# Optimization experiments

Measured on AMD Instinct MI355X. Metric: run time of the kernel, lower is better.

The kernel has to match this reference:

```python
import jax, jax.numpy as jnp
import numpy as np

B, T, V, H = 16, 256, 64, 256  # batch, time, num_inputs, hidden_dim
EPS = 1e-5

def _layernorm(h, g, b):
    mu = jnp.mean(h, axis=-1, keepdims=True)
    var = jnp.mean(jnp.square(h - mu), axis=-1, keepdims=True)
    return (h - mu) * jax.lax.rsqrt(var + EPS) * g + b

def setup_inputs() -> dict:
    key = jax.random.key(0)
    ks = jax.random.split(key, 16)
    s1, sH = 1.0, 1.0 / np.sqrt(H)
    sV = 1.0 / np.sqrt(V)
    inp = {
        "x": jax.random.normal(ks[0], (B, T, V), jnp.float32),
        # per-variable GRN params (input_dim=1), stacked over V
        "W1": jax.random.normal(ks[1], (V, H), jnp.float32) * s1,
        "b1": jnp.zeros((V, H), jnp.float32),
        "W2": jax.random.normal(ks[2], (V, H, H), jnp.float32) * sH,
        "b2": jnp.zeros((V, H), jnp.float32),
        "Wg": jax.random.normal(ks[3], (V, H), jnp.float32) * s1,  # first H rows of gate Linear(1,2H)
        "bg": jnp.zeros((V, H), jnp.float32),
        "Ws": jax.random.normal(ks[4], (V, H), jnp.float32) * s1,  # skip_proj Linear(1,H)
        "bs": jnp.zeros((V, H), jnp.float32),
        "g1": jnp.ones((V, H), jnp.float32),
        "be1": jnp.zeros((V, H), jnp.float32),
        # weight network GRN: V -> V, skip is Identity
        "nW1": jax.random.normal(ks[5], (V, V), jnp.float32) * sV,
        "nb1": jnp.zeros((V,), jnp.float32),
        "nW2": jax.random.normal(ks[6], (V, V), jnp.float32) * sV,
        "nb2": jnp.zeros((V,), jnp.float32),
        "nWg": jax.random.normal(ks[7], (V, V), jnp.float32) * sV,  # first V cols of gate Linear(V,2V)
        "nbg": jnp.zeros((V,), jnp.float32),
        "ng": jnp.ones((V,), jnp.float32),
        "nbe": jnp.zeros((V,), jnp.float32),
    }
    return inp

def reference(x, W1, b1, W2, b2, Wg, bg, Ws, bs, g1, be1,
              nW1, nb1, nW2, nb2, nWg, nbg, ng, nbe):
    # --- per-variable GRNs, vectorized over V (input is a scalar per variable) ---
    feat = x[..., None]                                     # [B,T,V,1]
    h1 = feat * W1 + b1                                     # [B,T,V,H]  fc1(1->H)
    res = jnp.einsum('btvh,vhk->btvk', jax.nn.elu(h1), W2) + b2  # fc2(H->H)
    gate = jax.nn.sigmoid(feat * Wg + bg)                   # gate(1->2H)[:H]
    skip = feat * Ws + bs                                   # skip_proj(1->H)
    var_out = _layernorm(skip + gate * res, g1, be1)        # [B,T,V,H]
    # --- weight network GRN on flattened input (V -> V, skip=Identity) ---
    wres = jnp.einsum('btv,vk->btk', jax.nn.elu(x @ nW1 + nb1), nW2) + nb2
    wgate = jax.nn.sigmoid(x @ nWg + nbg)
    wout = _layernorm(x + wgate * wres, ng, nbe)            # [B,T,V]
    weights = jax.nn.softmax(wout, axis=-1)                 # [B,T,V]
    combined = jnp.einsum('btvh,btv->bth', var_out, weights)  # [B,T,H]
    return combined
```

## Files before the change

### kernel.cpp

```cpp
#include <hip/hip_runtime.h>
#include <hip/hip_bf16.h>
#include <stdint.h>

#define NTOK 4096
#define NV 64
#define NH 256
#define LN_EPS 1e-5f

typedef __attribute__((ext_vector_type(8))) short short8;
typedef __attribute__((ext_vector_type(4))) float f32x4;
typedef __attribute__((ext_vector_type(4))) uint32_t u32x4;

__device__ __forceinline__ unsigned short f32_to_bf16(float f) {
    uint32_t u = __builtin_bit_cast(uint32_t, f);
    return (unsigned short)((u + 0x7FFFu + ((u >> 16) & 1u)) >> 16);
}
__device__ __forceinline__ float fsigmoid(float z) { return 1.0f / (1.0f + __expf(-z)); }
__device__ __forceinline__ float felu(float z) { return z > 0.0f ? z : (__expf(z) - 1.0f); }
__device__ __forceinline__ uint32_t pack_bf16x2(float ze, float zo) {
    const uint32_t ue = __builtin_bit_cast(uint32_t, ze) + 0x8000u;
    const uint32_t uo = __builtin_bit_cast(uint32_t, zo) + 0x8000u;
    return __builtin_amdgcn_perm(uo, ue, 0x07060302u);
}
__device__ __forceinline__ void gload16(const void* g, void* l) {
    __builtin_amdgcn_global_load_lds(
        (const __attribute__((address_space(1))) uint32_t*)g,
        (__attribute__((address_space(3))) uint32_t*)l, 16, 0, 0);
}

__global__ __launch_bounds__(256) void k_w2t(const float* __restrict__ W2,
                                             unsigned short* __restrict__ W2T) {
    __shared__ float tile[32][33];
    const int v  = blockIdx.x >> 6;
    const int t  = blockIdx.x & 63;
    const int h0 = (t & 7) * 32;
    const int o0 = (t >> 3) * 32;
    const int r  = threadIdx.x >> 3;
    const int c4 = (threadIdx.x & 7) * 4;
    const float4 d = *(const float4*)(W2 + ((size_t)v * NH + h0 + r) * NH + o0 + c4);
    tile[r][c4 + 0] = d.x; tile[r][c4 + 1] = d.y;
    tile[r][c4 + 2] = d.z; tile[r][c4 + 3] = d.w;
    __syncthreads();
    ushort4 o;
    o.x = f32_to_bf16(tile[c4 + 0][r]);
    o.y = f32_to_bf16(tile[c4 + 1][r]);
    o.z = f32_to_bf16(tile[c4 + 2][r]);
    o.w = f32_to_bf16(tile[c4 + 3][r]);
    *(ushort4*)(W2T + ((size_t)v * NH + o0 + r) * NH + h0 + c4) = o;
}

__global__ __launch_bounds__(256) void k_weights(
    const float* __restrict__ x,
    const float* __restrict__ nW1, const float* __restrict__ nb1,
    const float* __restrict__ nW2, const float* __restrict__ nb2,
    const float* __restrict__ nWg, const float* __restrict__ nbg,
    const float* __restrict__ ng,  const float* __restrict__ nbe,
    float* __restrict__ wout_buf) {
    const int wv = threadIdx.x >> 6;
    const int lane = threadIdx.x & 63;
    const int tok = blockIdx.x * 4 + wv;
    const float xv = x[(size_t)tok * NV + lane];
    float acc1 = nb1[lane], accg = nbg[lane];
#pragma unroll 8
    for (int k = 0; k < 64; ++k) {
        const float xk = __shfl(xv, k);
        acc1 = fmaf(xk, nW1[k * 64 + lane], acc1);
        accg = fmaf(xk, nWg[k * 64 + lane], accg);
    }
    const float h  = felu(acc1);
    const float wg = fsigmoid(accg);
    float acc2 = nb2[lane];
#pragma unroll 8
    for (int k = 0; k < 64; ++k) {
        const float hk = __shfl(h, k);
        acc2 = fmaf(hk, nW2[k * 64 + lane], acc2);
    }
    const float pre = xv + wg * acc2;
    float s = pre;
#pragma unroll
    for (int m = 32; m >= 1; m >>= 1) s += __shfl_xor(s, m);
    const float mu = s * (1.0f / 64.0f);
    const float dd = pre - mu;
    float s2 = dd * dd;
#pragma unroll
    for (int m = 32; m >= 1; m >>= 1) s2 += __shfl_xor(s2, m);
    const float inv = rsqrtf(s2 * (1.0f / 64.0f) + LN_EPS);
    const float wln = dd * inv * ng[lane] + nbe[lane];
    float mx = wln;
#pragma unroll
    for (int m = 32; m >= 1; m >>= 1) mx = fmaxf(mx, __shfl_xor(mx, m));
    const float e = __expf(wln - mx);
    float se = e;
#pragma unroll
    for (int m = 32; m >= 1; m >>= 1) se += __shfl_xor(se, m);
    wout_buf[(size_t)tok * NV + lane] = e / se;
}

__device__ __forceinline__ const float* row_ptr(int r, const float* W1, const float* b1,
                                                const float* Wg, const float* bg,
                                                const float* Ws, const float* bs,
                                                const float* b2, const float* g1,
                                                const float* be1) {
    switch (r) {
        case 0: return W1; case 1: return b1; case 2: return Wg; case 3: return bg;
        case 4: return Ws; case 5: return bs; case 6: return b2; case 7: return g1;
        default: return be1;
    }
}

__global__ __launch_bounds__(256, 2) void k_main(
    const float* __restrict__ x, const unsigned short* __restrict__ W2T,
    const float* __restrict__ W1, const float* __restrict__ b1,
    const float* __restrict__ Wg, const float* __restrict__ bg,
    const float* __restrict__ Ws, const float* __restrict__ bs,
    const float* __restrict__ b2, const float* __restrict__ g1,
    const float* __restrict__ be1, const float* __restrict__ wgts,
    float* __restrict__ partials,
    float* __restrict__ outacc) {
    __shared__ u32x4 sB[2][1024];
    __shared__ float sRB[2][9][256];
    __shared__ float sX[64][9];
    __shared__ float sW[64][9];

    const int tid  = threadIdx.x;
    const int wid  = tid >> 6, lane = tid & 63;
    const int c    = lane & 15, kg = lane >> 4;
    const int bid  = blockIdx.x;
    const int vg   = bid & 7, tt = bid >> 3;
    const int t0   = tt * 64, vbase = vg * 8;

    const float* r0p = row_ptr(2 * wid,     W1, b1, Wg, bg, Ws, bs, b2, g1, be1);
    const float* r1p = row_ptr(2 * wid + 1, W1, b1, Wg, bg, Ws, bs, b2, g1, be1);

    int bsrc[4], bdst[4];
#pragma unroll
    for (int q = 0; q < 4; ++q) {
        const int idx = wid * 256 + q * 64 + lane;
        const int o = idx >> 2, sl = idx & 3;
        const int s = (sl - (o >> 1)) & 3;
        bsrc[q] = o * NH + s * 8;
        bdst[q] = idx * 16;
    }

    const unsigned short* W2Tv0 = W2T + (size_t)vbase * (NH * NH);
    gload16(W2Tv0 + bsrc[0], (char*)sB[0] + bdst[0]);
    gload16(W2Tv0 + bsrc[1], (char*)sB[0] + bdst[1]);
    gload16(W2Tv0 + bsrc[2], (char*)sB[0] + bdst[2]);
    gload16(W2Tv0 + bsrc[3], (char*)sB[0] + bdst[3]);
    gload16(r0p + (size_t)vbase * NH + lane * 4, (char*)sRB[0] + (2 * wid) * 1024);
    gload16(r1p + (size_t)vbase * NH + lane * 4, (char*)sRB[0] + (2 * wid + 1) * 1024);
    if (wid == 0)
        gload16(be1 + (size_t)vbase * NH + lane * 4, (char*)sRB[0] + 8 * 1024);
#pragma unroll
    for (int e = 0; e < 2; ++e) {
        const int ee = tid + e * 256;
        const int row = ee >> 3, cc = ee & 7;
        sX[row][cc] = x[(size_t)(t0 + row) * NV + vbase + cc];
        sW[row][cc] = wgts[(size_t)(t0 + row) * NV + vbase + cc];
    }
    __syncthreads();

    const int rdbase = c * 64 + (((kg + (c >> 1)) & 3) << 4);
    const f32x4 fzero = {0.f, 0.f, 0.f, 0.f};

    f32x4 wacc[16];
#pragma unroll
    for (int f = 0; f < 16; ++f) wacc[f] = fzero;

#pragma unroll 1
    for (int vi = 0; vi < 8; ++vi) {
        const int rcur = vi & 1;
        const unsigned short* W2Tv = W2T + (size_t)(vbase + vi) * (NH * NH);
        const float xv = sX[wid * 16 + c][vi];

        f32x4 acc[16];
#pragma unroll
        for (int f = 0; f < 16; ++f) acc[f] = fzero;

#pragma unroll 1
        for (int ks = 0; ks < 8; ++ks) {
            const int cb = ks & 1;
            if (ks == 1 && vi < 7) {
                gload16(r0p + (size_t)(vbase + vi + 1) * NH + lane * 4,
                        (char*)sRB[rcur ^ 1] + (2 * wid) * 1024);
                gload16(r1p + (size_t)(vbase + vi + 1) * NH + lane * 4,
                        (char*)sRB[rcur ^ 1] + (2 * wid + 1) * 1024);
                if (wid == 0)
                    gload16(be1 + (size_t)(vbase + vi + 1) * NH + lane * 4,
                            (char*)sRB[rcur ^ 1] + 8 * 1024);
            }
            if (ks < 7 || vi < 7) {
                const unsigned short* Wsrc =
                    (ks < 7) ? (W2Tv + (ks + 1) * 32) : (W2Tv + NH * NH);
                char* bb1 = (char*)sB[cb ^ 1];
                gload16(Wsrc + bsrc[0], bb1 + bdst[0]);
                gload16(Wsrc + bsrc[1], bb1 + bdst[1]);
                gload16(Wsrc + bsrc[2], bb1 + bdst[2]);
                gload16(Wsrc + bsrc[3], bb1 + bdst[3]);
            }
            const int k0 = ks * 32 + kg * 8;
            const float4 wA = *(const float4*)&sRB[rcur][0][k0];
            const float4 wB = *(const float4*)&sRB[rcur][0][k0 + 4];
            const float4 bA = *(const float4*)&sRB[rcur][1][k0];
            const float4 bB = *(const float4*)&sRB[rcur][1][k0 + 4];
            u32x4 ap;
            {
                const float z0 = fmaf(xv, wA.x, bA.x), z1 = fmaf(xv, wA.y, bA.y);
                const float z2 = fmaf(xv, wA.z, bA.z), z3 = fmaf(xv, wA.w, bA.w);
                const float z4 = fmaf(xv, wB.x, bB.x), z5 = fmaf(xv, wB.y, bB.y);
                const float z6 = fmaf(xv, wB.z, bB.z), z7 = fmaf(xv, wB.w, bB.w);
                ap[0] = pack_bf16x2(felu(z0), felu(z1));
                ap[1] = pack_bf16x2(felu(z2), felu(z3));
                ap[2] = pack_bf16x2(felu(z4), felu(z5));
                ap[3] = pack_bf16x2(felu(z6), felu(z7));
            }
            const short8 af = __builtin_bit_cast(short8, ap);
            const char* bb = (const char*)sB[cb] + rdbase;
            __builtin_amdgcn_s_setprio(1);
#pragma unroll
            for (int f = 0; f < 16; ++f) {
                const short8 bf = __builtin_bit_cast(short8, *(const u32x4*)(bb + (f << 10)));
                acc[f] = __builtin_amdgcn_mfma_f32_16x16x32_bf16(af, bf, acc[f], 0, 0, 0);
            }
            __builtin_amdgcn_s_setprio(0);
            __syncthreads();
        }

        float xr[4], wv_[4];
#pragma unroll
        for (int r = 0; r < 4; ++r) {
            const int tl = wid * 16 + kg * 4 + r;
            xr[r]  = sX[tl][vi];
            wv_[r] = sW[tl][vi];
        }
        float ps[4] = {}, pq[4] = {};
        float gv[16], bev[16];
#pragma unroll
        for (int f = 0; f < 16; ++f) {
            const int h = f * 16 + c;
            const float Wg_ = sRB[rcur][2][h], bg_ = sRB[rcur][3][h];
            const float Ws_ = sRB[rcur][4][h], bs_ = sRB[rcur][5][h];
            const float b2_ = sRB[rcur][6][h];
            gv[f] = sRB[rcur][7][h]; bev[f] = sRB[rcur][8][h];
#pragma unroll
            for (int r = 0; r < 4; ++r) {
                const float y = fmaf(xr[r], Ws_, bs_) +
                                fsigmoid(fmaf(xr[r], Wg_, bg_)) * (acc[f][r] + b2_);
                acc[f][r] = y;
                ps[r] += y;
                pq[r] = fmaf(y, y, pq[r]);
            }
        }
#pragma unroll
        for (int m = 1; m <= 8; m <<= 1)
#pragma unroll
            for (int r = 0; r < 4; ++r) {
                ps[r] += __shfl_xor(ps[r], m);
                pq[r] += __shfl_xor(pq[r], m);
            }
#pragma unroll
        for (int r = 0; r < 4; ++r) {
            const float mu = ps[r] * (1.0f / 256.0f);
            const float vr = fmaf(-mu, mu, pq[r] * (1.0f / 256.0f));
            const float iv = rsqrtf(vr + LN_EPS);
            const float wiv = wv_[r] * iv;
#pragma unroll
            for (int f = 0; f < 16; ++f)
                wacc[f][r] = fmaf(wiv * (acc[f][r] - mu), gv[f],
                                  fmaf(wv_[r], bev[f], wacc[f][r]));
        }
    }

    const int tokb = t0 + wid * 16 + kg * 4;
    if (partials) {
        float* P = partials + (size_t)vg * NTOK * NH;
#pragma unroll
        for (int r = 0; r < 4; ++r) {
            float* rowp = P + (size_t)(tokb + r) * NH + c;
#pragma unroll
            for (int f = 0; f < 16; ++f) rowp[f * 16] = wacc[f][r];
        }
    } else {
#pragma unroll
        for (int r = 0; r < 4; ++r) {
            float* rowp = outacc + (size_t)(tokb + r) * NH + c;
#pragma unroll
            for (int f = 0; f < 16; ++f) atomicAdd(&rowp[f * 16], wacc[f][r]);
        }
    }
}

__global__ __launch_bounds__(256) void k_reduce(const float* __restrict__ P,
                                                float* __restrict__ out) {
    const size_t i = ((size_t)blockIdx.x * 256 + threadIdx.x);
    const f32x4* P4 = (const f32x4*)P;
    f32x4 s = P4[i];
#pragma unroll
    for (int sl = 1; sl < 8; ++sl) s += P4[(size_t)sl * (NTOK * NH / 4) + i];
    ((f32x4*)out)[i] = s;
}

extern "C" void kernel_launch(void* const* d_in, const int* in_sizes, int n_in,
                              void* d_out, int out_size, void* d_ws, size_t ws_size,
                              hipStream_t stream) {
    const float* x   = (const float*)d_in[0];
    const float* W1  = (const float*)d_in[1];
    const float* b1  = (const float*)d_in[2];
    const float* W2  = (const float*)d_in[3];
    const float* b2  = (const float*)d_in[4];
    const float* Wg  = (const float*)d_in[5];
    const float* bg  = (const float*)d_in[6];
    const float* Ws  = (const float*)d_in[7];
    const float* bs  = (const float*)d_in[8];
    const float* g1  = (const float*)d_in[9];
    const float* be1 = (const float*)d_in[10];
    const float* nW1 = (const float*)d_in[11];
    const float* nb1 = (const float*)d_in[12];
    const float* nW2 = (const float*)d_in[13];
    const float* nb2 = (const float*)d_in[14];
    const float* nWg = (const float*)d_in[15];
    const float* nbg = (const float*)d_in[16];
    const float* ng  = (const float*)d_in[17];
    const float* nbe = (const float*)d_in[18];
    float* out = (float*)d_out;

    char* ws = (char*)d_ws;
    float* ws_wgt = (float*)ws;
    unsigned short* ws_W2T = (unsigned short*)(ws + (1 << 20));
    const size_t part_off = (size_t)9 << 20;
    const size_t part_bytes = (size_t)8 * NTOK * NH * 4;
    const bool use_part = ws_size >= part_off + part_bytes;
    float* ws_part = use_part ? (float*)(ws + part_off) : nullptr;

    k_w2t<<<dim3(64 * 64), dim3(256), 0, stream>>>(W2, ws_W2T);
    k_weights<<<dim3(NTOK / 4), dim3(256), 0, stream>>>(x, nW1, nb1, nW2, nb2,
                                                        nWg, nbg, ng, nbe, ws_wgt);
    if (!use_part) hipMemsetAsync(d_out, 0, (size_t)out_size * 4, stream);
    k_main<<<dim3(512), dim3(256), 0, stream>>>(x, ws_W2T, W1, b1, Wg, bg, Ws, bs,
                                                b2, g1, be1, ws_wgt, ws_part, out);
    if (use_part)
        k_reduce<<<dim3(NTOK * NH / 4 / 256), dim3(256), 0, stream>>>(ws_part, out);
}
```

Before: 143.5 us.

## Load W2 fragments directly into registers, drop LDS staging and barriers

The W2 prep kernel now writes bf16 weights already arranged in MFMA B-fragment order, so the main kernel reads them straight from global memory into registers. It double-buffers them as two halves (bLo/bHi) instead of staging through LDS with global_load_lds and a barrier per k-step. x and the softmax weights are now stored token-contiguous (an extra transpose kernel for x) so vector loads replace the shared-memory tiles. Per-variable parameters are read from global/L2 on demand instead of being prefetched into LDS. This removes LDS traffic and syncs but increases register pressure and depends on the cache for repeated weight reads.

```diff
diff --git a/kernel.cpp b/kernel.cpp
--- a/kernel.cpp
+++ b/kernel.cpp
@@ -22,31 +22,46 @@
     const uint32_t uo = __builtin_bit_cast(uint32_t, zo) + 0x8000u;
     return __builtin_amdgcn_perm(uo, ue, 0x07060302u);
 }
-__device__ __forceinline__ void gload16(const void* g, void* l) {
-    __builtin_amdgcn_global_load_lds(
-        (const __attribute__((address_space(1))) uint32_t*)g,
-        (__attribute__((address_space(3))) uint32_t*)l, 16, 0, 0);
-}
-
-__global__ __launch_bounds__(256) void k_w2t(const float* __restrict__ W2,
-                                             unsigned short* __restrict__ W2T) {
-    __shared__ float tile[32][33];
+
+__global__ __launch_bounds__(128) void k_w2f(const float* __restrict__ W2,
+                                             unsigned short* __restrict__ W2F) {
+    __shared__ float tile[32][36];
     const int v  = blockIdx.x >> 6;
     const int t  = blockIdx.x & 63;
-    const int h0 = (t & 7) * 32;
+    const int ks = t & 7;
     const int o0 = (t >> 3) * 32;
-    const int r  = threadIdx.x >> 3;
-    const int c4 = (threadIdx.x & 7) * 4;
-    const float4 d = *(const float4*)(W2 + ((size_t)v * NH + h0 + r) * NH + o0 + c4);
-    tile[r][c4 + 0] = d.x; tile[r][c4 + 1] = d.y;
-    tile[r][c4 + 2] = d.z; tile[r][c4 + 3] = d.w;
+    const int r  = threadIdx.x >> 2;
+    const int c8 = (threadIdx.x & 3) * 8;
+    const float* src = W2 + ((size_t)v * NH + ks * 32 + r) * NH + o0 + c8;
+    *(float4*)&tile[r][c8]     = *(const float4*)src;
+    *(float4*)&tile[r][c8 + 4] = *(const float4*)(src + 4);
     __syncthreads();
-    ushort4 o;
-    o.x = f32_to_bf16(tile[c4 + 0][r]);
-    o.y = f32_to_bf16(tile[c4 + 1][r]);
-    o.z = f32_to_bf16(tile[c4 + 2][r]);
-    o.w = f32_to_bf16(tile[c4 + 3][r]);
-    *(ushort4*)(W2T + ((size_t)v * NH + o0 + r) * NH + h0 + c4) = o;
+    const int fi = threadIdx.x >> 6;
+    const int l  = threadIdx.x & 63;
+    const int cc = l & 15, kg = l >> 4;
+    const int f  = (o0 >> 4) + fi;
+    u32x4 w;
+#pragma unroll
+    for (int p = 0; p < 4; ++p) {
+        const float z0 = tile[kg * 8 + 2 * p][fi * 16 + cc];
+        const float z1 = tile[kg * 8 + 2 * p + 1][fi * 16 + cc];
+        w[p] = (uint32_t)f32_to_bf16(z0) | ((uint32_t)f32_to_bf16(z1) << 16);
+    }
+    *(u32x4*)(W2F + ((size_t)(((v * 8 + ks) * 16) + f) * 64 + l) * 8) = w;
+}
+
+__global__ __launch_bounds__(256) void k_xt(const float* __restrict__ x,
+                                            float* __restrict__ xT) {
+    __shared__ float tile[64][65];
+    const int t0 = blockIdx.x * 64;
+    const int r = threadIdx.x >> 2, q = threadIdx.x & 3;
+#pragma unroll
+    for (int j = 0; j < 16; ++j)
+        tile[r][q * 16 + j] = x[(size_t)(t0 + r) * NV + q * 16 + j];
+    __syncthreads();
+#pragma unroll
+    for (int j = 0; j < 16; ++j)
+        xT[(size_t)r * NTOK + t0 + q * 16 + j] = tile[q * 16 + j][r];
 }
 
 __global__ __launch_bounds__(256) void k_weights(
@@ -55,7 +70,7 @@
     const float* __restrict__ nW2, const float* __restrict__ nb2,
     const float* __restrict__ nWg, const float* __restrict__ nbg,
     const float* __restrict__ ng,  const float* __restrict__ nbe,
-    float* __restrict__ wout_buf) {
+    float* __restrict__ wT) {
     const int wv = threadIdx.x >> 6;
     const int lane = threadIdx.x & 63;
     const int tok = blockIdx.x * 4 + wv;
@@ -93,85 +108,49 @@
     float se = e;
 #pragma unroll
     for (int m = 32; m >= 1; m >>= 1) se += __shfl_xor(se, m);
-    wout_buf[(size_t)tok * NV + lane] = e / se;
-}
-
-__device__ __forceinline__ const float* row_ptr(int r, const float* W1, const float* b1,
-                                                const float* Wg, const float* bg,
-                                                const float* Ws, const float* bs,
-                                                const float* b2, const float* g1,
-                                                const float* be1) {
-    switch (r) {
-        case 0: return W1; case 1: return b1; case 2: return Wg; case 3: return bg;
-        case 4: return Ws; case 5: return bs; case 6: return b2; case 7: return g1;
-        default: return be1;
-    }
-}
+    wT[(size_t)lane * NTOK + tok] = e / se;
+}
+
+#define LOADH(dst, basep, fb)                                               \
+    {                                                                       \
+        _Pragma("unroll") for (int j_ = 0; j_ < 8; ++j_)                    \
+            dst[j_] = *(const u32x4*)((basep) + ((fb) + j_) * 1024 + loff); \
+    }
 
 __global__ __launch_bounds__(256, 2) void k_main(
-    const float* __restrict__ x, const unsigned short* __restrict__ W2T,
+    const char* __restrict__ W2F, const float* __restrict__ xT,
+    const float* __restrict__ wT,
     const float* __restrict__ W1, const float* __restrict__ b1,
     const float* __restrict__ Wg, const float* __restrict__ bg,
     const float* __restrict__ Ws, const float* __restrict__ bs,
     const float* __restrict__ b2, const float* __restrict__ g1,
-    const float* __restrict__ be1, const float* __restrict__ wgts,
+    const float* __restrict__ be1,
     float* __restrict__ partials,
     float* __restrict__ outacc) {
-    __shared__ u32x4 sB[2][1024];
-    __shared__ float sRB[2][9][256];
-    __shared__ float sX[64][9];
-    __shared__ float sW[64][9];
-
     const int tid  = threadIdx.x;
     const int wid  = tid >> 6, lane = tid & 63;
     const int c    = lane & 15, kg = lane >> 4;
-    const int bid  = blockIdx.x;
-    const int vg   = bid & 7, tt = bid >> 3;
+    const int vg   = blockIdx.x & 7, tt = blockIdx.x >> 3;
     const int t0   = tt * 64, vbase = vg * 8;
-
-    const float* r0p = row_ptr(2 * wid,     W1, b1, Wg, bg, Ws, bs, b2, g1, be1);
-    const float* r1p = row_ptr(2 * wid + 1, W1, b1, Wg, bg, Ws, bs, b2, g1, be1);
-
-    int bsrc[4], bdst[4];
-#pragma unroll
-    for (int q = 0; q < 4; ++q) {
-        const int idx = wid * 256 + q * 64 + lane;
-        const int o = idx >> 2, sl = idx & 3;
-        const int s = (sl - (o >> 1)) & 3;
-        bsrc[q] = o * NH + s * 8;
-        bdst[q] = idx * 16;
-    }
-
-    const unsigned short* W2Tv0 = W2T + (size_t)vbase * (NH * NH);
-    gload16(W2Tv0 + bsrc[0], (char*)sB[0] + bdst[0]);
-    gload16(W2Tv0 + bsrc[1], (char*)sB[0] + bdst[1]);
-    gload16(W2Tv0 + bsrc[2], (char*)sB[0] + bdst[2]);
-    gload16(W2Tv0 + bsrc[3], (char*)sB[0] + bdst[3]);
-    gload16(r0p + (size_t)vbase * NH + lane * 4, (char*)sRB[0] + (2 * wid) * 1024);
-    gload16(r1p + (size_t)vbase * NH + lane * 4, (char*)sRB[0] + (2 * wid + 1) * 1024);
-    if (wid == 0)
-        gload16(be1 + (size_t)vbase * NH + lane * 4, (char*)sRB[0] + 8 * 1024);
-#pragma unroll
-    for (int e = 0; e < 2; ++e) {
-        const int ee = tid + e * 256;
-        const int row = ee >> 3, cc = ee & 7;
-        sX[row][cc] = x[(size_t)(t0 + row) * NV + vbase + cc];
-        sW[row][cc] = wgts[(size_t)(t0 + row) * NV + vbase + cc];
-    }
-    __syncthreads();
-
-    const int rdbase = c * 64 + (((kg + (c >> 1)) & 3) << 4);
+    const int tw   = t0 + wid * 16;
+    const int loff = lane * 16;
+
     const f32x4 fzero = {0.f, 0.f, 0.f, 0.f};
-
     f32x4 wacc[16];
 #pragma unroll
     for (int f = 0; f < 16; ++f) wacc[f] = fzero;
+
+    u32x4 bLo[8], bHi[8];
+    const char* pv = W2F + (size_t)vbase * 131072;
+    LOADH(bLo, pv, 0);
 
 #pragma unroll 1
     for (int vi = 0; vi < 8; ++vi) {
-        const int rcur = vi & 1;
-        const unsigned short* W2Tv = W2T + (size_t)(vbase + vi) * (NH * NH);
-        const float xv = sX[wid * 16 + c][vi];
+        const int v = vbase + vi;
+        const char* pvn = pv + 131072;
+        const float xa = xT[(size_t)v * NTOK + tw + c];
+        const float4 xr4 = *(const float4*)&xT[(size_t)v * NTOK + tw + kg * 4];
+        const float4 wr4 = *(const float4*)&wT[(size_t)v * NTOK + tw + kg * 4];
 
         f32x4 acc[16];
 #pragma unroll
@@ -179,69 +158,55 @@
 
 #pragma unroll 1
         for (int ks = 0; ks < 8; ++ks) {
-            const int cb = ks & 1;
-            if (ks == 1 && vi < 7) {
-                gload16(r0p + (size_t)(vbase + vi + 1) * NH + lane * 4,
-                        (char*)sRB[rcur ^ 1] + (2 * wid) * 1024);
-                gload16(r1p + (size_t)(vbase + vi + 1) * NH + lane * 4,
-                        (char*)sRB[rcur ^ 1] + (2 * wid + 1) * 1024);
-                if (wid == 0)
-                    gload16(be1 + (size_t)(vbase + vi + 1) * NH + lane * 4,
-                            (char*)sRB[rcur ^ 1] + 8 * 1024);
-            }
-            if (ks < 7 || vi < 7) {
-                const unsigned short* Wsrc =
-                    (ks < 7) ? (W2Tv + (ks + 1) * 32) : (W2Tv + NH * NH);
-                char* bb1 = (char*)sB[cb ^ 1];
-                gload16(Wsrc + bsrc[0], bb1 + bdst[0]);
-                gload16(Wsrc + bsrc[1], bb1 + bdst[1]);
-                gload16(Wsrc + bsrc[2], bb1 + bdst[2]);
-                gload16(Wsrc + bsrc[3], bb1 + bdst[3]);
-            }
-            const int k0 = ks * 32 + kg * 8;
-            const float4 wA = *(const float4*)&sRB[rcur][0][k0];
-            const float4 wB = *(const float4*)&sRB[rcur][0][k0 + 4];
-            const float4 bA = *(const float4*)&sRB[rcur][1][k0];
-            const float4 bB = *(const float4*)&sRB[rcur][1][k0 + 4];
+            const char* pk = pv + ks * 16384;
+            LOADH(bHi, pk, 8);
+            const float* w1p = W1 + (size_t)v * NH + ks * 32 + kg * 8;
+            const float* b1p = b1 + (size_t)v * NH + ks * 32 + kg * 8;
+            const float4 wA = *(const float4*)w1p;
+            const float4 wB = *(const float4*)(w1p + 4);
+            const float4 bA = *(const float4*)b1p;
+            const float4 bB = *(const float4*)(b1p + 4);
             u32x4 ap;
             {
-                const float z0 = fmaf(xv, wA.x, bA.x), z1 = fmaf(xv, wA.y, bA.y);
-                const float z2 = fmaf(xv, wA.z, bA.z), z3 = fmaf(xv, wA.w, bA.w);
-                const float z4 = fmaf(xv, wB.x, bB.x), z5 = fmaf(xv, wB.y, bB.y);
-                const float z6 = fmaf(xv, wB.z, bB.z), z7 = fmaf(xv, wB.w, bB.w);
+                const float z0 = fmaf(xa, wA.x, bA.x), z1 = fmaf(xa, wA.y, bA.y);
+                const float z2 = fmaf(xa, wA.z, bA.z), z3 = fmaf(xa, wA.w, bA.w);
+                const float z4 = fmaf(xa, wB.x, bB.x), z5 = fmaf(xa, wB.y, bB.y);
+                const float z6 = fmaf(xa, wB.z, bB.z), z7 = fmaf(xa, wB.w, bB.w);
                 ap[0] = pack_bf16x2(felu(z0), felu(z1));
                 ap[1] = pack_bf16x2(felu(z2), felu(z3));
                 ap[2] = pack_bf16x2(felu(z4), felu(z5));
                 ap[3] = pack_bf16x2(felu(z6), felu(z7));
             }
             const short8 af = __builtin_bit_cast(short8, ap);
-            const char* bb = (const char*)sB[cb] + rdbase;
             __builtin_amdgcn_s_setprio(1);
 #pragma unroll
-            for (int f = 0; f < 16; ++f) {
-                const short8 bf = __builtin_bit_cast(short8, *(const u32x4*)(bb + (f << 10)));
-                acc[f] = __builtin_amdgcn_mfma_f32_16x16x32_bf16(af, bf, acc[f], 0, 0, 0);
+            for (int f = 0; f < 8; ++f)
+                acc[f] = __builtin_amdgcn_mfma_f32_16x16x32_bf16(
+                    af, __builtin_bit_cast(short8, bLo[f]), acc[f], 0, 0, 0);
+            __builtin_amdgcn_s_setprio(0);
+            if (ks < 7) {
+                LOADH(bLo, pk + 16384, 0);
+            } else if (vi < 7) {
+                LOADH(bLo, pvn, 0);
             }
+            __builtin_amdgcn_s_setprio(1);
+#pragma unroll
+            for (int f = 0; f < 8; ++f)
+                acc[8 + f] = __builtin_amdgcn_mfma_f32_16x16x32_bf16(
+                    af, __builtin_bit_cast(short8, bHi[f]), acc[8 + f], 0, 0, 0);
             __builtin_amdgcn_s_setprio(0);
-            __syncthreads();
-        }
-
-        float xr[4], wv_[4];
-#pragma unroll
-        for (int r = 0; r < 4; ++r) {
-            const int tl = wid * 16 + kg * 4 + r;
-            xr[r]  = sX[tl][vi];
-            wv_[r] = sW[tl][vi];
-        }
+        }
+        pv = pvn;
+
+        const float xr[4] = {xr4.x, xr4.y, xr4.z, xr4.w};
+        const float wv_[4] = {wr4.x, wr4.y, wr4.z, wr4.w};
         float ps[4] = {}, pq[4] = {};
-        float gv[16], bev[16];
+        const size_t vro = (size_t)v * NH + c;
 #pragma unroll
         for (int f = 0; f < 16; ++f) {
-            const int h = f * 16 + c;
-            const float Wg_ = sRB[rcur][2][h], bg_ = sRB[rcur][3][h];
-            const float Ws_ = sRB[rcur][4][h], bs_ = sRB[rcur][5][h];
-            const float b2_ = sRB[rcur][6][h];
-            gv[f] = sRB[rcur][7][h]; bev[f] = sRB[rcur][8][h];
+            const float Wg_ = Wg[vro + f * 16], bg_ = bg[vro + f * 16];
+            const float Ws_ = Ws[vro + f * 16], bs_ = bs[vro + f * 16];
+            const float b2_ = b2[vro + f * 16];
 #pragma unroll
             for (int r = 0; r < 4; ++r) {
                 const float y = fmaf(xr[r], Ws_, bs_) +
@@ -258,16 +223,20 @@
                 ps[r] += __shfl_xor(ps[r], m);
                 pq[r] += __shfl_xor(pq[r], m);
             }
+        float mu[4], wiv[4];
 #pragma unroll
         for (int r = 0; r < 4; ++r) {
-            const float mu = ps[r] * (1.0f / 256.0f);
-            const float vr = fmaf(-mu, mu, pq[r] * (1.0f / 256.0f));
-            const float iv = rsqrtf(vr + LN_EPS);
-            const float wiv = wv_[r] * iv;
-#pragma unroll
-            for (int f = 0; f < 16; ++f)
-                wacc[f][r] = fmaf(wiv * (acc[f][r] - mu), gv[f],
-                                  fmaf(wv_[r], bev[f], wacc[f][r]));
+            mu[r] = ps[r] * (1.0f / 256.0f);
+            const float vr = fmaf(-mu[r], mu[r], pq[r] * (1.0f / 256.0f));
+            wiv[r] = wv_[r] * rsqrtf(vr + LN_EPS);
+        }
+#pragma unroll
+        for (int f = 0; f < 16; ++f) {
+            const float g1_ = g1[vro + f * 16], be_ = be1[vro + f * 16];
+#pragma unroll
+            for (int r = 0; r < 4; ++r)
+                wacc[f][r] = fmaf(wiv[r] * (acc[f][r] - mu[r]), g1_,
+                                  fmaf(wv_[r], be_, wacc[f][r]));
         }
     }
 
@@ -325,19 +294,22 @@
     float* out = (float*)d_out;
 
     char* ws = (char*)d_ws;
-    float* ws_wgt = (float*)ws;
-    unsigned short* ws_W2T = (unsigned short*)(ws + (1 << 20));
-    const size_t part_off = (size_t)9 << 20;
+    float* ws_wT  = (float*)ws;
+    float* ws_xT  = (float*)(ws + (1 << 20));
+    unsigned short* ws_W2F = (unsigned short*)(ws + (2 << 20));
+    const size_t part_off = (size_t)10 << 20;
     const size_t part_bytes = (size_t)8 * NTOK * NH * 4;
     const bool use_part = ws_size >= part_off + part_bytes;
     float* ws_part = use_part ? (float*)(ws + part_off) : nullptr;
 
-    k_w2t<<<dim3(64 * 64), dim3(256), 0, stream>>>(W2, ws_W2T);
+    k_w2f<<<dim3(64 * 64), dim3(128), 0, stream>>>(W2, ws_W2F);
+    k_xt<<<dim3(NTOK / 64), dim3(256), 0, stream>>>(x, ws_xT);
     k_weights<<<dim3(NTOK / 4), dim3(256), 0, stream>>>(x, nW1, nb1, nW2, nb2,
-                                                        nWg, nbg, ng, nbe, ws_wgt);
+                                                        nWg, nbg, ng, nbe, ws_wT);
     if (!use_part) hipMemsetAsync(d_out, 0, (size_t)out_size * 4, stream);
-    k_main<<<dim3(512), dim3(256), 0, stream>>>(x, ws_W2T, W1, b1, Wg, bg, Ws, bs,
-                                                b2, g1, be1, ws_wgt, ws_part, out);
+    k_main<<<dim3(512), dim3(256), 0, stream>>>((const char*)ws_W2F, ws_xT, ws_wT,
+                                                W1, b1, Wg, bg, Ws, bs, b2, g1, be1,
+                                                ws_part, out);
     if (use_part)
         k_reduce<<<dim3(NTOK * NH / 4 / 256), dim3(256), 0, stream>>>(ws_part, out);
 }
```

After: 185.6 us. 1.29x slower.

## Triple-buffer W2 tiles with prefetch distance two and one barrier per step

Applied to the files above, without the earlier changes.

The shared-memory B buffer grows from two to three stages so W2 tiles are prefetched two k-steps ahead. The per-row parameter loads move into the same pipeline, issued alongside the first tile of the next variable. The end-of-step __syncthreads is replaced by an explicit vmcnt wait plus a single s_barrier at the top of each step, and the next loads are issued after that barrier. This aims to hide global-load latency and cut synchronization stalls, at the cost of 16KB more LDS per block, which may limit occupancy, and more fragile wait-count reasoning.

```diff
diff --git a/kernel.cpp b/kernel.cpp
--- a/kernel.cpp
+++ b/kernel.cpp
@@ -117,7 +117,7 @@
     const float* __restrict__ be1, const float* __restrict__ wgts,
     float* __restrict__ partials,
     float* __restrict__ outacc) {
-    __shared__ u32x4 sB[2][1024];
+    __shared__ u32x4 sB[3][1024];
     __shared__ float sRB[2][9][256];
     __shared__ float sX[64][9];
     __shared__ float sW[64][9];
@@ -142,15 +142,30 @@
         bdst[q] = idx * 16;
     }
 
-    const unsigned short* W2Tv0 = W2T + (size_t)vbase * (NH * NH);
-    gload16(W2Tv0 + bsrc[0], (char*)sB[0] + bdst[0]);
-    gload16(W2Tv0 + bsrc[1], (char*)sB[0] + bdst[1]);
-    gload16(W2Tv0 + bsrc[2], (char*)sB[0] + bdst[2]);
-    gload16(W2Tv0 + bsrc[3], (char*)sB[0] + bdst[3]);
-    gload16(r0p + (size_t)vbase * NH + lane * 4, (char*)sRB[0] + (2 * wid) * 1024);
-    gload16(r1p + (size_t)vbase * NH + lane * 4, (char*)sRB[0] + (2 * wid + 1) * 1024);
-    if (wid == 0)
-        gload16(be1 + (size_t)vbase * NH + lane * 4, (char*)sRB[0] + 8 * 1024);
+#define STAGE_B(vt, kt, buf)                                                     \
+    do {                                                                         \
+        const unsigned short* Wsrc_ = W2T + (size_t)(vt) * (NH * NH) + (kt) * 32;\
+        char* dst_ = (char*)sB[buf];                                             \
+        gload16(Wsrc_ + bsrc[0], dst_ + bdst[0]);                                \
+        gload16(Wsrc_ + bsrc[1], dst_ + bdst[1]);                                \
+        gload16(Wsrc_ + bsrc[2], dst_ + bdst[2]);                                \
+        gload16(Wsrc_ + bsrc[3], dst_ + bdst[3]);                                \
+    } while (0)
+
+#define STAGE_ROWS(vt, rbuf)                                                     \
+    do {                                                                         \
+        gload16(r0p + (size_t)(vt) * NH + lane * 4,                              \
+                (char*)sRB[rbuf] + (2 * wid) * 1024);                            \
+        gload16(r1p + (size_t)(vt) * NH + lane * 4,                              \
+                (char*)sRB[rbuf] + (2 * wid + 1) * 1024);                        \
+        if (wid == 0)                                                            \
+            gload16(be1 + (size_t)(vt) * NH + lane * 4,                          \
+                    (char*)sRB[rbuf] + 8 * 1024);                                \
+    } while (0)
+
+    STAGE_B(vbase, 0, 0);
+    STAGE_B(vbase, 1, 1);
+    STAGE_ROWS(vbase, 0);
 #pragma unroll
     for (int e = 0; e < 2; ++e) {
         const int ee = tid + e * 256;
@@ -167,10 +182,11 @@
 #pragma unroll
     for (int f = 0; f < 16; ++f) wacc[f] = fzero;
 
+    int cur = 0;
+
 #pragma unroll 1
     for (int vi = 0; vi < 8; ++vi) {
         const int rcur = vi & 1;
-        const unsigned short* W2Tv = W2T + (size_t)(vbase + vi) * (NH * NH);
         const float xv = sX[wid * 16 + c][vi];
 
         f32x4 acc[16];
@@ -179,25 +195,10 @@
 
 #pragma unroll 1
         for (int ks = 0; ks < 8; ++ks) {
-            const int cb = ks & 1;
-            if (ks == 1 && vi < 7) {
-                gload16(r0p + (size_t)(vbase + vi + 1) * NH + lane * 4,
-                        (char*)sRB[rcur ^ 1] + (2 * wid) * 1024);
-                gload16(r1p + (size_t)(vbase + vi + 1) * NH + lane * 4,
-                        (char*)sRB[rcur ^ 1] + (2 * wid + 1) * 1024);
-                if (wid == 0)
-                    gload16(be1 + (size_t)(vbase + vi + 1) * NH + lane * 4,
-                            (char*)sRB[rcur ^ 1] + 8 * 1024);
-            }
-            if (ks < 7 || vi < 7) {
-                const unsigned short* Wsrc =
-                    (ks < 7) ? (W2Tv + (ks + 1) * 32) : (W2Tv + NH * NH);
-                char* bb1 = (char*)sB[cb ^ 1];
-                gload16(Wsrc + bsrc[0], bb1 + bdst[0]);
-                gload16(Wsrc + bsrc[1], bb1 + bdst[1]);
-                gload16(Wsrc + bsrc[2], bb1 + bdst[2]);
-                gload16(Wsrc + bsrc[3], bb1 + bdst[3]);
-            }
+            asm volatile("s_waitcnt vmcnt(4)" ::: "memory");
+            __builtin_amdgcn_sched_barrier(0);
+            __builtin_amdgcn_s_barrier();
+
             const int k0 = ks * 32 + kg * 8;
             const float4 wA = *(const float4*)&sRB[rcur][0][k0];
             const float4 wB = *(const float4*)&sRB[rcur][0][k0 + 4];
@@ -214,8 +215,19 @@
                 ap[2] = pack_bf16x2(felu(z4), felu(z5));
                 ap[3] = pack_bf16x2(felu(z6), felu(z7));
             }
+
+            {
+                const int nxt2 = (cur == 0) ? 2 : cur - 1;
+                if (ks < 6) {
+                    STAGE_B(vbase + vi, ks + 2, nxt2);
+                } else if (vi < 7) {
+                    STAGE_B(vbase + vi + 1, ks - 6, nxt2);
+                    if (ks == 6) STAGE_ROWS(vbase + vi + 1, rcur ^ 1);
+                }
+            }
+
             const short8 af = __builtin_bit_cast(short8, ap);
-            const char* bb = (const char*)sB[cb] + rdbase;
+            const char* bb = (const char*)sB[cur] + rdbase;
             __builtin_amdgcn_s_setprio(1);
 #pragma unroll
             for (int f = 0; f < 16; ++f) {
@@ -223,7 +235,7 @@
                 acc[f] = __builtin_amdgcn_mfma_f32_16x16x32_bf16(af, bf, acc[f], 0, 0, 0);
             }
             __builtin_amdgcn_s_setprio(0);
-            __syncthreads();
+            cur = (cur == 2) ? 0 : cur + 1;
         }
 
         float xr[4], wv_[4];
@@ -270,6 +282,8 @@
                                   fmaf(wv_[r], bev[f], wacc[f][r]));
         }
     }
+#undef STAGE_B
+#undef STAGE_ROWS
 
     const int tokb = t0 + wid * 16 + kg * 4;
     if (partials) {
```

After: 141.3 us. Within noise of the previous version (-1.5%).
